# Optimization experiments

Measured on AMD Instinct MI355X. Metric: run time of the kernel, lower is better.

Reference implementation:

```python
import jax, jax.numpy as jnp
import numpy as np
import math

B, SQ, SK, HEADS, DH = 4, 4096, 308, 8, 64
INNER = HEADS * DH


def setup_inputs() -> dict:
    key = jax.random.key(0)
    k1, k2, k3, k4, k5 = jax.random.split(key, 5)
    q = jax.random.normal(k1, (B, SQ, INNER), dtype=jnp.float32)
    k = jax.random.normal(k2, (B, SK, INNER), dtype=jnp.float32)
    v = jax.random.normal(k3, (B, SK, INNER), dtype=jnp.float32)
    # mask_scale: positive multiplicative rescale (H*W / mask_area in original)
    mask_scale = jax.random.uniform(k4, (B, HEADS, SQ, SK), dtype=jnp.float32) + 0.5
    # mask_bool: region membership mask (masks > 0.5 in original)
    mask_bool = jax.random.randint(k5, (B, HEADS, SQ, SK), 0, 2) > 0
    return {"q": q, "k": k, "v": v, "mask_scale": mask_scale,
            "mask_bool": mask_bool, "heads": HEADS}


def reference(q, k, v, mask_scale, mask_bool, heads):
    b, sq, inner = q.shape
    dh = inner // heads
    # (b, s, h*dh) -> (b, h, s, dh)
    def split_heads(t):
        return t.reshape(b, -1, heads, dh).transpose(0, 2, 1, 3)
    qh, kh, vh = split_heads(q), split_heads(k), split_heads(v)
    scores = jnp.einsum('bhqd,bhkd->bhqk', qh, kh) / math.sqrt(dh)
    scores = scores * mask_scale
    scores = jnp.where(mask_bool, scores, -jnp.inf)
    attn = jax.nn.softmax(scores, axis=-1)
    out = jnp.einsum('bhqk,bhkd->bhqd', attn, vh)
    # (b, h, q, dh) -> (b, q, h*dh)
    return out.transpose(0, 2, 1, 3).reshape(b, sq, heads * dh)
```

## Files before the change

kernel.cpp:

```cpp
#include <hip/hip_runtime.h>


#define NB     4
#define NSQ    4096
#define NSK    308
#define NH     8
#define NDH    64
#define NINNER 512
#define NKT    20
#define QBLK   32
#define NTHREADS 128
#define NCH    (QBLK*NSK/4)

#define KFRAG_PER_BH (NKT*2*64*8)
#define VFRAG_PER_BH (NKT*64*16)
#define WS_BYTES ((size_t)(NB*NH) * (KFRAG_PER_BH + VFRAG_PER_BH) * 2)

typedef _Float16 h8 __attribute__((ext_vector_type(8)));
typedef _Float16 h4 __attribute__((ext_vector_type(4)));
typedef float    f4 __attribute__((ext_vector_type(4)));
typedef int      i4 __attribute__((ext_vector_type(4)));

__global__ __launch_bounds__(512) void omost_prep(
    const float* __restrict__ Kg, const float* __restrict__ Vg,
    _Float16* __restrict__ ws)
{
  const int bh  = blockIdx.x;
  const int b   = bh >> 3;
  const int h   = bh & 7;
  const int tid = threadIdx.x;

  _Float16* Kfrag = ws + (size_t)bh * KFRAG_PER_BH;
  _Float16* Vfrag = ws + (size_t)(NB*NH) * KFRAG_PER_BH + (size_t)bh * VFRAG_PER_BH;

  const float* Kb = Kg + (size_t)b * NSK * NINNER + h * NDH;
  #pragma unroll
  for (int i = 0; i < (NKT*2*64) / 512; ++i) {
    int s   = tid + i * 512;
    int l   = s & 63;
    int dhc = (s >> 6) & 1;
    int kt  = s >> 7;
    int row = kt * 16 + (l & 15);
    int col = dhc * 32 + ((l >> 4) << 3);
    h8 hk;
    #pragma unroll
    for (int j = 0; j < 8; ++j) hk[j] = (_Float16)0.f;
    if (row < NSK) {
      const float* p = Kb + (size_t)row * NINNER + col;
      f4 a = *(const f4*)p;
      f4 c = *(const f4*)(p + 4);
      hk[0]=(_Float16)a[0]; hk[1]=(_Float16)a[1]; hk[2]=(_Float16)a[2]; hk[3]=(_Float16)a[3];
      hk[4]=(_Float16)c[0]; hk[5]=(_Float16)c[1]; hk[6]=(_Float16)c[2]; hk[7]=(_Float16)c[3];
    }
    *(h8*)(Kfrag + (size_t)s * 8) = hk;
  }

  const float* Vb = Vg + (size_t)b * NSK * NINNER + h * NDH;
  #pragma unroll
  for (int i = 0; i < 3; ++i) {
    int s = tid + i * 512;
    if (s < NKT * 64) {
      int l    = s & 63;
      int kt   = s >> 6;
      int row0 = kt * 16 + ((l >> 4) << 2);
      int colb = l & 15;
      h8 lo, hi;
      #pragma unroll
      for (int nt = 0; nt < 2; ++nt)
        #pragma unroll
        for (int j = 0; j < 4; ++j) {
          int row = row0 + j;
          lo[nt*4+j] = (row < NSK) ? (_Float16)Vb[(size_t)row * NINNER + nt*16 + colb]
                                   : (_Float16)0.f;
        }
      #pragma unroll
      for (int nt = 2; nt < 4; ++nt)
        #pragma unroll
        for (int j = 0; j < 4; ++j) {
          int row = row0 + j;
          hi[(nt-2)*4+j] = (row < NSK) ? (_Float16)Vb[(size_t)row * NINNER + nt*16 + colb]
                                       : (_Float16)0.f;
        }
      *(h8*)(Vfrag + (size_t)s * 16)     = lo;
      *(h8*)(Vfrag + (size_t)s * 16 + 8) = hi;
    }
  }
}

__global__ __launch_bounds__(NTHREADS) void omost_attn(
    const float* __restrict__ Qg, const float* __restrict__ MSg,
    const int*   __restrict__ MBg, const _Float16* __restrict__ ws,
    float* __restrict__ Og)
{
  __shared__ __align__(16) _Float16 Mlds[QBLK * NSK];

  const int tid  = threadIdx.x;
  const int lane = tid & 63;
  const int wv   = tid >> 6;
  const int lg   = lane >> 4;
  const int lr   = lane & 15;

  const int wg = blockIdx.x;
  const int qt = wg & (NSQ / QBLK - 1);
  const int bh = wg >> 7;
  const int b  = bh >> 3;
  const int h  = bh & 7;

  const int q0   = qt * QBLK + wv * 16;
  const int qrow = q0 + lr;

  const h8* Kf = (const h8*)(ws + (size_t)bh * KFRAG_PER_BH);
  const h8* Vf = (const h8*)(ws + (size_t)(NB*NH) * KFRAG_PER_BH + (size_t)bh * VFRAG_PER_BH);

  const float* Qb = Qg + ((size_t)b * NSQ + qrow) * NINNER + h * NDH;
  f4 qraw0 = __builtin_nontemporal_load((const f4*)(Qb + lg * 8));
  f4 qraw1 = __builtin_nontemporal_load((const f4*)(Qb + lg * 8 + 4));
  f4 qraw2 = __builtin_nontemporal_load((const f4*)(Qb + 32 + lg * 8));
  f4 qraw3 = __builtin_nontemporal_load((const f4*)(Qb + 32 + lg * 8 + 4));

  const size_t mbase = ((size_t)bh * NSQ + qt * QBLK) * NSK;
  #pragma unroll
  for (int g = 0; g < 2; ++g) {
    f4 msr[10]; i4 mbr[10];
    #pragma unroll
    for (int j = 0; j < 10; ++j) {
      int cc  = tid + (g * 10 + j) * NTHREADS;
      int ccl = cc < NCH ? cc : NCH - 1;
      msr[j] = __builtin_nontemporal_load((const f4*)(MSg + mbase + 4 * (size_t)ccl));
      mbr[j] = __builtin_nontemporal_load((const i4*)(MBg + mbase + 4 * (size_t)ccl));
    }
    #pragma unroll
    for (int j = 0; j < 10; ++j) {
      int cc = tid + (g * 10 + j) * NTHREADS;
      if (cc < NCH) {
        h4 fm;
        #pragma unroll
        for (int r = 0; r < 4; ++r)
          fm[r] = (mbr[j][r] != 0) ? (_Float16)msr[j][r] : (_Float16)0.f;
        *(h4*)(&Mlds[4 * cc]) = fm;
      }
    }
  }
  __syncthreads();

  h8 qf0, qf1;
  {
    qf0[0]=(_Float16)(qraw0[0]*0.125f); qf0[1]=(_Float16)(qraw0[1]*0.125f);
    qf0[2]=(_Float16)(qraw0[2]*0.125f); qf0[3]=(_Float16)(qraw0[3]*0.125f);
    qf0[4]=(_Float16)(qraw1[0]*0.125f); qf0[5]=(_Float16)(qraw1[1]*0.125f);
    qf0[6]=(_Float16)(qraw1[2]*0.125f); qf0[7]=(_Float16)(qraw1[3]*0.125f);
    qf1[0]=(_Float16)(qraw2[0]*0.125f); qf1[1]=(_Float16)(qraw2[1]*0.125f);
    qf1[2]=(_Float16)(qraw2[2]*0.125f); qf1[3]=(_Float16)(qraw2[3]*0.125f);
    qf1[4]=(_Float16)(qraw3[0]*0.125f); qf1[5]=(_Float16)(qraw3[1]*0.125f);
    qf1[6]=(_Float16)(qraw3[2]*0.125f); qf1[7]=(_Float16)(qraw3[3]*0.125f);
  }

  const int mlrow = (wv * 16 + lr) * NSK;
  f4 acc0 = {0.f,0.f,0.f,0.f}, acc1 = {0.f,0.f,0.f,0.f};
  f4 acc2 = {0.f,0.f,0.f,0.f}, acc3 = {0.f,0.f,0.f,0.f};
  float ssum = 0.f;

#define MK_KBL(kt_) ((kt_) * 16 + lg * 4 > (NSK - 4) ? (NSK - 4) : (kt_) * 16 + lg * 4)

#define COMPUTE(kt_, k0_, k1_, vlo_, vhi_, m_)                                   \
  do {                                                                           \
    const int kb_ = (kt_) * 16 + lg * 4;                                         \
    f4 c_ = {0.f, 0.f, 0.f, 0.f};                                                \
    c_ = __builtin_amdgcn_mfma_f32_16x16x32_f16((k0_), qf0, c_, 0, 0, 0);        \
    c_ = __builtin_amdgcn_mfma_f32_16x16x32_f16((k1_), qf1, c_, 0, 0, 0);        \
    h4 pa_;                                                                      \
    _Pragma("unroll")                                                            \
    for (int r = 0; r < 4; ++r) {                                                \
      float mf_ = (float)(m_)[r];                                                \
      bool ok_ = (kb_ + r < NSK) && (mf_ != 0.f);                                \
      float p_ = ok_ ? __expf(__builtin_fmaf(c_[r], mf_, -4.f)) : 0.f;           \
      ssum += p_;                                                                \
      pa_[r] = (_Float16)p_;                                                     \
    }                                                                            \
    h4 v0_ = {(vlo_)[0], (vlo_)[1], (vlo_)[2], (vlo_)[3]};                       \
    h4 v1_ = {(vlo_)[4], (vlo_)[5], (vlo_)[6], (vlo_)[7]};                       \
    h4 v2_ = {(vhi_)[0], (vhi_)[1], (vhi_)[2], (vhi_)[3]};                       \
    h4 v3_ = {(vhi_)[4], (vhi_)[5], (vhi_)[6], (vhi_)[7]};                       \
    acc0 = __builtin_amdgcn_mfma_f32_16x16x16f16(pa_, v0_, acc0, 0, 0, 0);       \
    acc1 = __builtin_amdgcn_mfma_f32_16x16x16f16(pa_, v1_, acc1, 0, 0, 0);       \
    acc2 = __builtin_amdgcn_mfma_f32_16x16x16f16(pa_, v2_, acc2, 0, 0, 0);       \
    acc3 = __builtin_amdgcn_mfma_f32_16x16x16f16(pa_, v3_, acc3, 0, 0, 0);       \
  } while (0)

  h8 kA0 = Kf[0 * 64 + lane], kA1 = Kf[1 * 64 + lane];
  h8 vAlo = Vf[(0 * 64 + lane) * 2], vAhi = Vf[(0 * 64 + lane) * 2 + 1];
  h4 mA  = *(const h4*)(&Mlds[mlrow + MK_KBL(0)]);
  h8 kB0, kB1, vBlo, vBhi; h4 mB;

  #pragma unroll
  for (int p = 0; p < NKT / 2; ++p) {
    const int ktB = 2 * p + 1;
    kB0  = Kf[(ktB * 2 + 0) * 64 + lane];
    kB1  = Kf[(ktB * 2 + 1) * 64 + lane];
    vBlo = Vf[(ktB * 64 + lane) * 2];
    vBhi = Vf[(ktB * 64 + lane) * 2 + 1];
    mB   = *(const h4*)(&Mlds[mlrow + MK_KBL(ktB)]);
    COMPUTE(2 * p, kA0, kA1, vAlo, vAhi, mA);
    const int ktA = (2 * p + 2 < NKT) ? (2 * p + 2) : (NKT - 1);
    kA0  = Kf[(ktA * 2 + 0) * 64 + lane];
    kA1  = Kf[(ktA * 2 + 1) * 64 + lane];
    vAlo = Vf[(ktA * 64 + lane) * 2];
    vAhi = Vf[(ktA * 64 + lane) * 2 + 1];
    mA   = *(const h4*)(&Mlds[mlrow + MK_KBL(ktA)]);
    COMPUTE(2 * p + 1, kB0, kB1, vBlo, vBhi, mB);
  }
#undef COMPUTE
#undef MK_KBL

  ssum += __shfl_xor(ssum, 16, 64);
  ssum += __shfl_xor(ssum, 32, 64);
  const float inv = 1.f / fmaxf(ssum, 1e-30f);

  float invr[4];
  #pragma unroll
  for (int r = 0; r < 4; ++r) invr[r] = __shfl(inv, lg * 4 + r, 64);

  float* Ob = Og + (size_t)b * NSQ * NINNER + h * NDH;
  f4 accs[4] = {acc0, acc1, acc2, acc3};
  #pragma unroll
  for (int nt = 0; nt < 4; ++nt) {
    #pragma unroll
    for (int r = 0; r < 4; ++r) {
      int qq = q0 + lg * 4 + r;
      __builtin_nontemporal_store(accs[nt][r] * invr[r],
                                  &Ob[(size_t)qq * NINNER + nt * 16 + lr]);
    }
  }
}

extern "C" void kernel_launch(void* const* d_in, const int* in_sizes, int n_in,
                              void* d_out, int out_size, void* d_ws, size_t ws_size,
                              hipStream_t stream) {
  const float* Qg  = (const float*)d_in[0];
  const float* Kg  = (const float*)d_in[1];
  const float* Vg  = (const float*)d_in[2];
  const float* MSg = (const float*)d_in[3];
  const int*   MBg = (const int*)d_in[4];
  float* Og = (float*)d_out;
  _Float16* ws = (_Float16*)d_ws;

  if (ws_size < WS_BYTES) return;

  omost_prep<<<dim3(NB*NH), dim3(512), 0, stream>>>(Kg, Vg, ws);

  const int nwg = NB * NH * (NSQ / QBLK);
  omost_attn<<<dim3(nwg), dim3(NTHREADS), 0, stream>>>(Qg, MSg, MBg, ws, Og);
}
```

Baseline: 100.6 us.

## Stream mask scale and bool directly into LDS via global_load_lds

Mask scale and mask bool tiles are now copied from global memory straight into LDS with 16-byte global_load_lds, instead of being loaded into registers, merged into one fp16 value and stored to LDS. The inner loop then reads fp32 scale and int bool separately from LDS and applies the mask there. The goal is to remove the register staging and conversion work and free VGPRs. In exchange, LDS per block grows about fourfold (to roughly 79 KB of dynamic shared memory), which sharply limits resident blocks per CU. It also doubles the LDS read traffic in the main loop.

After: 102.1 us. No clear change (+1.5%).

```diff
diff --git a/kernel.cpp b/kernel.cpp
--- a/kernel.cpp
+++ b/kernel.cpp
@@ -11,10 +11,13 @@
 #define QBLK   32
 #define NTHREADS 128
 #define NCH    (QBLK*NSK/4)
+#define NELEM  (QBLK*NSK)
 
 #define KFRAG_PER_BH (NKT*2*64*8)
 #define VFRAG_PER_BH (NKT*64*16)
 #define WS_BYTES ((size_t)(NB*NH) * (KFRAG_PER_BH + VFRAG_PER_BH) * 2)
+
+#define LDS_BYTES (NELEM * 8)
 
 typedef _Float16 h8 __attribute__((ext_vector_type(8)));
 typedef _Float16 h4 __attribute__((ext_vector_type(4)));
@@ -92,7 +95,9 @@
     const int*   __restrict__ MBg, const _Float16* __restrict__ ws,
     float* __restrict__ Og)
 {
-  __shared__ __align__(16) _Float16 Mlds[QBLK * NSK];
+  extern __shared__ __align__(16) float smem[];
+  float* MsL = smem;
+  int*   MbL = (int*)(smem + NELEM);
 
   const int tid  = threadIdx.x;
   const int lane = tid & 63;
@@ -119,25 +124,21 @@
   f4 qraw3 = __builtin_nontemporal_load((const f4*)(Qb + 32 + lg * 8 + 4));
 
   const size_t mbase = ((size_t)bh * NSQ + qt * QBLK) * NSK;
-  #pragma unroll
-  for (int g = 0; g < 2; ++g) {
-    f4 msr[10]; i4 mbr[10];
+  {
+    const float* msg = MSg + mbase;
+    const int*   mbg = MBg + mbase;
     #pragma unroll
-    for (int j = 0; j < 10; ++j) {
-      int cc  = tid + (g * 10 + j) * NTHREADS;
-      int ccl = cc < NCH ? cc : NCH - 1;
-      msr[j] = __builtin_nontemporal_load((const f4*)(MSg + mbase + 4 * (size_t)ccl));
-      mbr[j] = __builtin_nontemporal_load((const i4*)(MBg + mbase + 4 * (size_t)ccl));
-    }
-    #pragma unroll
-    for (int j = 0; j < 10; ++j) {
-      int cc = tid + (g * 10 + j) * NTHREADS;
+    for (int j = 0; j < 20; ++j) {
+      int cc = tid + j * NTHREADS;
       if (cc < NCH) {
-        h4 fm;
-        #pragma unroll
-        for (int r = 0; r < 4; ++r)
-          fm[r] = (mbr[j][r] != 0) ? (_Float16)msr[j][r] : (_Float16)0.f;
-        *(h4*)(&Mlds[4 * cc]) = fm;
+        __builtin_amdgcn_global_load_lds(
+            (const __attribute__((address_space(1))) unsigned int*)(msg + 4 * (size_t)cc),
+            (__attribute__((address_space(3))) unsigned int*)(MsL + 4 * (size_t)(j * NTHREADS + wv * 64)),
+            16, 0, 2 );
+        __builtin_amdgcn_global_load_lds(
+            (const __attribute__((address_space(1))) unsigned int*)(mbg + 4 * (size_t)cc),
+            (__attribute__((address_space(3))) unsigned int*)((float*)MbL + 4 * (size_t)(j * NTHREADS + wv * 64)),
+            16, 0, 2 );
       }
     }
   }
@@ -162,7 +163,7 @@
 
 #define MK_KBL(kt_) ((kt_) * 16 + lg * 4 > (NSK - 4) ? (NSK - 4) : (kt_) * 16 + lg * 4)
 
-#define COMPUTE(kt_, k0_, k1_, vlo_, vhi_, m_)                                   \
+#define COMPUTE(kt_, k0_, k1_, vlo_, vhi_, ms_, mb_)                             \
   do {                                                                           \
     const int kb_ = (kt_) * 16 + lg * 4;                                         \
     f4 c_ = {0.f, 0.f, 0.f, 0.f};                                                \
@@ -171,9 +172,8 @@
     h4 pa_;                                                                      \
     _Pragma("unroll")                                                            \
     for (int r = 0; r < 4; ++r) {                                                \
-      float mf_ = (float)(m_)[r];                                                \
-      bool ok_ = (kb_ + r < NSK) && (mf_ != 0.f);                                \
-      float p_ = ok_ ? __expf(__builtin_fmaf(c_[r], mf_, -4.f)) : 0.f;           \
+      bool ok_ = (kb_ + r < NSK) && ((mb_)[r] != 0);                             \
+      float p_ = ok_ ? __expf(__builtin_fmaf(c_[r], (ms_)[r], -4.f)) : 0.f;      \
       ssum += p_;                                                                \
       pa_[r] = (_Float16)p_;                                                     \
     }                                                                            \
@@ -189,8 +189,9 @@
 
   h8 kA0 = Kf[0 * 64 + lane], kA1 = Kf[1 * 64 + lane];
   h8 vAlo = Vf[(0 * 64 + lane) * 2], vAhi = Vf[(0 * 64 + lane) * 2 + 1];
-  h4 mA  = *(const h4*)(&Mlds[mlrow + MK_KBL(0)]);
-  h8 kB0, kB1, vBlo, vBhi; h4 mB;
+  f4 msA = *(const f4*)(&MsL[mlrow + MK_KBL(0)]);
+  i4 mbA = *(const i4*)(&MbL[mlrow + MK_KBL(0)]);
+  h8 kB0, kB1, vBlo, vBhi; f4 msB; i4 mbB;
 
   #pragma unroll
   for (int p = 0; p < NKT / 2; ++p) {
@@ -199,15 +200,17 @@
     kB1  = Kf[(ktB * 2 + 1) * 64 + lane];
     vBlo = Vf[(ktB * 64 + lane) * 2];
     vBhi = Vf[(ktB * 64 + lane) * 2 + 1];
-    mB   = *(const h4*)(&Mlds[mlrow + MK_KBL(ktB)]);
-    COMPUTE(2 * p, kA0, kA1, vAlo, vAhi, mA);
+    msB  = *(const f4*)(&MsL[mlrow + MK_KBL(ktB)]);
+    mbB  = *(const i4*)(&MbL[mlrow + MK_KBL(ktB)]);
+    COMPUTE(2 * p, kA0, kA1, vAlo, vAhi, msA, mbA);
     const int ktA = (2 * p + 2 < NKT) ? (2 * p + 2) : (NKT - 1);
     kA0  = Kf[(ktA * 2 + 0) * 64 + lane];
     kA1  = Kf[(ktA * 2 + 1) * 64 + lane];
     vAlo = Vf[(ktA * 64 + lane) * 2];
     vAhi = Vf[(ktA * 64 + lane) * 2 + 1];
-    mA   = *(const h4*)(&Mlds[mlrow + MK_KBL(ktA)]);
-    COMPUTE(2 * p + 1, kB0, kB1, vBlo, vBhi, mB);
+    msA  = *(const f4*)(&MsL[mlrow + MK_KBL(ktA)]);
+    mbA  = *(const i4*)(&MbL[mlrow + MK_KBL(ktA)]);
+    COMPUTE(2 * p + 1, kB0, kB1, vBlo, vBhi, msB, mbB);
   }
 #undef COMPUTE
 #undef MK_KBL
@@ -246,8 +249,12 @@
 
   if (ws_size < WS_BYTES) return;
 
+  static_assert(LDS_BYTES <= 160 * 1024, "exceeds gfx950 LDS");
+  (void)hipFuncSetAttribute((const void*)omost_attn,
+                            hipFuncAttributeMaxDynamicSharedMemorySize, LDS_BYTES);
+
   omost_prep<<<dim3(NB*NH), dim3(512), 0, stream>>>(Kg, Vg, ws);
 
   const int nwg = NB * NH * (NSQ / QBLK);
-  omost_attn<<<dim3(nwg), dim3(NTHREADS), 0, stream>>>(Qg, MSg, MBg, ws, Og);
+  omost_attn<<<dim3(nwg), dim3(NTHREADS), LDS_BYTES, stream>>>(Qg, MSg, MBg, ws, Og);
 }
```
